# Performance work log

Measured on AMD Instinct MI355X. Metric: run time of the kernel, lower is better.

The kernel has to match this reference:

```python
import jax, jax.numpy as jnp
import numpy as np

ENT_TOTAL = 100000
REL_TOTAL = 1000
HIDDEN = 128
BATCH_SEQ = 8192  # 2 * batch_size (pos + neg halves)
MARGIN = 1.0
LAMB = 0.01
REG = 0.01


def setup_inputs() -> dict:
    key = jax.random.key(0)
    k0, k1, k2 = jax.random.split(key, 3)
    # [batch_seq, 3] index triples (h, r, t); values valid for both tables
    inp = jax.random.randint(k0, (BATCH_SEQ, 3), 0, REL_TOTAL, dtype=jnp.int64)
    # xavier-ish embedding tables
    scale = 1.0 / np.sqrt(HIDDEN)
    ent_emb = jax.random.normal(k1, (ENT_TOTAL, HIDDEN), dtype=jnp.float32) * scale
    rel_emb = jax.random.normal(k2, (REL_TOTAL, HIDDEN), dtype=jnp.float32) * scale
    Wr = jnp.zeros((REL_TOTAL, HIDDEN, HIDDEN), dtype=jnp.float32)
    return {"input": inp, "ent_emb": ent_emb, "rel_emb": rel_emb, "Wr": Wr}


def reference(input, ent_emb, rel_emb, Wr):
    bs = input.shape[0] // 2
    # gather embeddings (torch code keeps a singleton middle dim; we squeeze it)
    h = ent_emb[input[:, 0]]  # [2bs, H]
    r = rel_emb[input[:, 1]]
    t = ent_emb[input[:, 2]]
    error = jnp.abs(h + r - t)  # [2bs, H]
    ep, en = error[:bs], error[bs:]

    # relWr[b] = en_b en_b^T - ep_b ep_b^T  (abs-error outer products)
    relWr = jnp.einsum('bh,bk->bhk', en, en) - jnp.einsum('bh,bk->bhk', ep, ep)

    # matching torch scatter_ nondeterministic overwrite semantics)
    pos_r = input[:bs, 1]
    Wr_new = Wr.at[pos_r].set(relWr)

    # quadratic-form cross scores: p[i, j] = ep_i^T relWr_j ep_j (torch broadcast matmul semantics)
    vp = jnp.einsum('jhk,jk->jh', relWr, ep)  # [bs, H]
    vn = jnp.einsum('jhk,jk->jh', relWr, en)
    p_score = ep @ vp.T  # [bs, bs]
    n_score = en @ vn.T

    margin_loss = jnp.sum(jax.nn.relu(p_score - n_score + MARGIN)) / bs
    wr_loss = jnp.linalg.norm(relWr.reshape(-1)) * LAMB  # Frobenius (p=2) norm
    norm_loss = (jnp.linalg.norm(h.reshape(-1)) + jnp.linalg.norm(r.reshape(-1))
                 + jnp.linalg.norm(t.reshape(-1))) * REG
    loss = margin_loss + wr_loss + norm_loss
    return (loss, Wr_new)
```

## Files before the change

### kernel.cpp

```cpp
#include <hip/hip_runtime.h>
#include <hip/hip_bf16.h>
#include <math.h>

#define HID 128
#define BSEQ 8192
#define BSH 4096
#define RELS 1000
#define KEXT 256

typedef unsigned int u32;
typedef __attribute__((ext_vector_type(8))) short bf16x8;
typedef __attribute__((ext_vector_type(4))) float f32x4;


__device__ inline unsigned short f2bf(float x) {
    u32 u = __float_as_uint(x);
    u32 r = (u + 0x7fff + ((u >> 16) & 1)) >> 16;
    return (unsigned short)r;
}

__device__ inline u32 pack2bf(float x) {
    unsigned short hi = f2bf(x);
    float hf = __uint_as_float((u32)hi << 16);
    unsigned short lo = f2bf(x - hf);
    return (u32)hi | ((u32)lo << 16);
}

#define GLOAD_LDS16(g, l) __builtin_amdgcn_global_load_lds( \
    (const __attribute__((address_space(1))) u32*)(g), \
    (__attribute__((address_space(3))) u32*)(l), 16, 0, 0)

__global__ void k_init(int* __restrict__ winner) {
    int t = blockIdx.x * blockDim.x + threadIdx.x;
    if (t < RELS) winner[t] = -1;
}

__global__ __launch_bounds__(256) void k_prep(const int* __restrict__ idx,
                                              const float* __restrict__ ent,
                                              const float* __restrict__ rel,
                                              float* __restrict__ e,
                                              u32* __restrict__ S,
                                              float* __restrict__ abc,
                                              int* __restrict__ winner,
                                              double* __restrict__ part) {
    const int b = blockIdx.x;
    const int half = threadIdx.x >> 7;
    const int k = threadIdx.x & 127;
    const int row = half ? (b + BSH) : b;
    const int i0 = idx[row * 3 + 0];
    const int i1 = idx[row * 3 + 1];
    const int i2 = idx[row * 3 + 2];
    const float h = ent[(size_t)i0 * HID + k];
    const float r = rel[(size_t)i1 * HID + k];
    const float t = ent[(size_t)i2 * HID + k];
    const float val = fabsf(h + r - t);
    e[(size_t)row * HID + k] = val;

    __shared__ float sE[2][128];
    __shared__ float sh[3][4];
    __shared__ float sPart[3][2];
    sE[half][k] = val;

    float hh = h * h, rr = r * r, tt = t * t;
    #pragma unroll
    for (int off = 32; off; off >>= 1) {
        hh += __shfl_down(hh, off);
        rr += __shfl_down(rr, off);
        tt += __shfl_down(tt, off);
    }
    int lane = threadIdx.x & 63, wv = threadIdx.x >> 6;
    if (lane == 0) { sh[0][wv] = hh; sh[1][wv] = rr; sh[2][wv] = tt; }
    __syncthreads();

    const float p = sE[0][k], n = sE[1][k];
    {
        size_t base = ((size_t)(1 + half) * BSH + b) * (KEXT / 2);
        S[base + k] = pack2bf(val);
        if (half == 0) {
            size_t ub = (size_t)b * (KEXT / 2);
            S[ub + k] = pack2bf(p + n);
        }
    }
    if (half == 0) {
        float ak = p * n, bk = p * p, ck = n * n;
        #pragma unroll
        for (int off = 32; off; off >>= 1) {
            ak += __shfl_down(ak, off);
            bk += __shfl_down(bk, off);
            ck += __shfl_down(ck, off);
        }
        if (lane == 0) { sPart[0][wv] = ak; sPart[1][wv] = bk; sPart[2][wv] = ck; }
    }
    __syncthreads();
    if (threadIdx.x == 0) {
        float a = sPart[0][0] + sPart[0][1];
        float bb = sPart[1][0] + sPart[1][1];
        float c = sPart[2][0] + sPart[2][1];
        abc[b] = a; abc[BSH + b] = bb; abc[2 * BSH + b] = c;
        double ad = a, bd = bb, cd = c;
        part[(size_t)b * 4 + 0] = (double)(sh[0][0] + sh[0][1] + sh[0][2] + sh[0][3]);
        part[(size_t)b * 4 + 1] = (double)(sh[1][0] + sh[1][1] + sh[1][2] + sh[1][3]);
        part[(size_t)b * 4 + 2] = (double)(sh[2][0] + sh[2][1] + sh[2][2] + sh[2][3]);
        part[(size_t)b * 4 + 3] = cd * cd - 2.0 * ad * ad + bd * bd;
        atomicMax(&winner[i1], b);
    }
}

__global__ __launch_bounds__(256) void k_scoremm(const unsigned short* __restrict__ S,
                                                 const float* __restrict__ abc,
                                                 double* __restrict__ pm) {
    int bi = blockIdx.y, bj = blockIdx.x;
    const int flat = bi * 64 + bj;
    if (bj < bi) {
        if (threadIdx.x == 0) pm[flat] = 0.0;
        return;
    }
    const int I0 = bi * 64, J0 = bj * 64;
    __shared__ __align__(16) unsigned short sAll[6 * 64 * 32];
    __shared__ float sRed[4];
    const int t = threadIdx.x;
    const int lane = t & 63, wv = t >> 6;
    const int wr = wv >> 1, wc = wv & 1;
    const int lam = lane & 15, lag = lane >> 4;

    f32x4 a0[2][2] = {}, a1[2][2] = {}, a2[2][2] = {};

    for (int kc = 0; kc < 8; ++kc) {
        __syncthreads();
        #pragma unroll
        for (int qq = 0; qq < 6; ++qq) {
            int q = wv * 6 + qq;
            int b = q * 1024 + lane * 16;
            int arr = b >> 12;
            int within = b & 4095;
            int row = within >> 6;
            int colB = within & 63;
            int m = arr >> 1;
            int R0 = (arr & 1) ? J0 : I0;
            const unsigned short* src = S + ((size_t)(m * BSH + R0 + row) << 8)
                                          + kc * 32 + (colB >> 1);
            GLOAD_LDS16(src, &sAll[q * 512]);
        }
        __syncthreads();
        bf16x8 fa[3][2], fb[3][2];
        #pragma unroll
        for (int m = 0; m < 3; ++m) {
            #pragma unroll
            for (int f = 0; f < 2; ++f) {
                fa[m][f] = *(const bf16x8*)&sAll[(m * 2 + 0) * 2048
                              + (wr * 32 + f * 16 + lam) * 32 + lag * 8];
                fb[m][f] = *(const bf16x8*)&sAll[(m * 2 + 1) * 2048
                              + (wc * 32 + f * 16 + lam) * 32 + lag * 8];
            }
        }
        #pragma unroll
        for (int fi = 0; fi < 2; ++fi)
            #pragma unroll
            for (int fj = 0; fj < 2; ++fj) {
                a0[fi][fj] = __builtin_amdgcn_mfma_f32_16x16x32_bf16(fa[0][fi], fb[0][fj], a0[fi][fj], 0, 0, 0);
                a1[fi][fj] = __builtin_amdgcn_mfma_f32_16x16x32_bf16(fa[1][fi], fb[1][fj], a1[fi][fj], 0, 0, 0);
                a2[fi][fj] = __builtin_amdgcn_mfma_f32_16x16x32_bf16(fa[2][fi], fb[2][fj], a2[fi][fj], 0, 0, 0);
            }
    }

    const float* A = abc;
    const float* Bv = abc + BSH;
    const float* Cv = abc + 2 * BSH;
    float lsum = 0.f;
    #pragma unroll
    for (int fj = 0; fj < 2; ++fj) {
        int j = J0 + wc * 32 + fj * 16 + lam;
        float aj = A[j], abj = aj + Bv[j], acj = aj + Cv[j];
        #pragma unroll
        for (int fi = 0; fi < 2; ++fi)
            #pragma unroll
            for (int r = 0; r < 4; ++r) {
                float s = fmaf(aj, a0[fi][fj][r], 1.0f)
                          - abj * a1[fi][fj][r] - acj * a2[fi][fj][r];
                lsum += fmaxf(s, 0.f);
            }
    }
    if (bj != bi) {
        #pragma unroll
        for (int fi = 0; fi < 2; ++fi)
            #pragma unroll
            for (int r = 0; r < 4; ++r) {
                int i = I0 + wr * 32 + fi * 16 + lag * 4 + r;
                float ai = A[i], abi = ai + Bv[i], aci = ai + Cv[i];
                #pragma unroll
                for (int fj = 0; fj < 2; ++fj) {
                    float s = fmaf(ai, a0[fi][fj][r], 1.0f)
                              - abi * a1[fi][fj][r] - aci * a2[fi][fj][r];
                    lsum += fmaxf(s, 0.f);
                }
            }
    }
    #pragma unroll
    for (int off = 32; off; off >>= 1) lsum += __shfl_down(lsum, off);
    if (lane == 0) sRed[wv] = lsum;
    __syncthreads();
    if (t == 0)
        pm[flat] = (double)(sRed[0] + sRed[1] + sRed[2] + sRed[3]);
}

__global__ __launch_bounds__(256) void k_reduce(const double* __restrict__ pp,
                                                const double* __restrict__ pm,
                                                float* __restrict__ out) {
    int t = threadIdx.x;
    double h2 = 0, r2 = 0, t2 = 0, wr = 0, mg = 0;
    for (int i = t; i < BSH; i += 256) {
        h2 += pp[(size_t)i * 4 + 0];
        r2 += pp[(size_t)i * 4 + 1];
        t2 += pp[(size_t)i * 4 + 2];
        wr += pp[(size_t)i * 4 + 3];
        mg += pm[i];
    }
    #pragma unroll
    for (int off = 32; off; off >>= 1) {
        h2 += __shfl_down(h2, off);
        r2 += __shfl_down(r2, off);
        t2 += __shfl_down(t2, off);
        wr += __shfl_down(wr, off);
        mg += __shfl_down(mg, off);
    }
    __shared__ double sred[5][4];
    int lane = t & 63, wv = t >> 6;
    if (lane == 0) {
        sred[0][wv] = h2; sred[1][wv] = r2; sred[2][wv] = t2;
        sred[3][wv] = wr; sred[4][wv] = mg;
    }
    __syncthreads();
    if (t == 0) {
        double H = sred[0][0] + sred[0][1] + sred[0][2] + sred[0][3];
        double R = sred[1][0] + sred[1][1] + sred[1][2] + sred[1][3];
        double T = sred[2][0] + sred[2][1] + sred[2][2] + sred[2][3];
        double W = sred[3][0] + sred[3][1] + sred[3][2] + sred[3][3];
        double M = sred[4][0] + sred[4][1] + sred[4][2] + sred[4][3];
        out[0] = (float)(M / (double)BSH + sqrt(W) * 0.01
                         + (sqrt(H) + sqrt(R) + sqrt(T)) * 0.01);
    }
}

__global__ __launch_bounds__(256) void k_wrout(const float* __restrict__ Wr,
                                               const float* __restrict__ e,
                                               const int* __restrict__ winner,
                                               float* __restrict__ outWr) {
    int rel = blockIdx.x;
    int t = threadIdx.x;
    float* out = outWr + (size_t)rel * HID * HID;
    int j = winner[rel];
    if (j < 0) {
        const float* src = Wr + (size_t)rel * HID * HID;
        #pragma unroll 8
        for (int it = 0; it < 64; ++it) out[it * 256 + t] = src[it * 256 + t];
    } else {
        __shared__ float sep[HID], sen[HID];
        if (t < 128) sep[t] = e[(size_t)j * HID + t];
        else sen[t - 128] = e[(size_t)(j + BSH) * HID + (t - 128)];
        __syncthreads();
        #pragma unroll 8
        for (int it = 0; it < 64; ++it) {
            int ix = it * 256 + t;
            int hh = ix >> 7, kk = ix & 127;
            out[ix] = sen[hh] * sen[kk] - sep[hh] * sep[kk];
        }
    }
}

extern "C" void kernel_launch(void* const* d_in, const int* in_sizes, int n_in,
                              void* d_out, int out_size, void* d_ws, size_t ws_size,
                              hipStream_t stream) {
    const int* idx = (const int*)d_in[0];
    const float* ent = (const float*)d_in[1];
    const float* rel = (const float*)d_in[2];
    const float* Wr = (const float*)d_in[3];
    float* out = (float*)d_out;

    char* ws = (char*)d_ws;
    int* winner = (int*)(ws + 64);
    float* abc = (float*)(ws + 4096);
    float* e = (float*)(ws + 53248);
    u32* S = (u32*)(out + 4);
    double* pp = (double*)((char*)d_out + 6291488);
    double* pm = (double*)((char*)d_out + 6422560);

    k_init<<<4, 256, 0, stream>>>(winner);
    k_prep<<<BSH, 256, 0, stream>>>(idx, ent, rel, e, S, abc, winner, pp);
    k_scoremm<<<dim3(64, 64), 256, 0, stream>>>((const unsigned short*)S, abc, pm);
    k_reduce<<<1, 256, 0, stream>>>(pp, pm, out);
    k_wrout<<<RELS, 256, 0, stream>>>(Wr, e, winner, out + 1);
}
```

Before: 222.6 us.

## Double-buffer LDS staging in score matmul and launch only upper-triangle tiles

The score GEMM kernel now stages K-chunks into two LDS buffers with explicit vmcnt waits, so the global-to-LDS loads for chunk k+2 overlap the MFMA work on chunk k. The grid is also shrunk from a 64x64 launch, where lower-triangle blocks exited immediately, to a 1D launch of only the 2080 upper-triangle tiles. Each tile's row and column are recovered with a sqrt-based index mapping, and the final reduction reads only those 2080 partials. This doubles LDS use per block and relies on hand-placed waitcnt and barrier ordering for correctness.

Measured after the change: 212.3 us. -4.6%, faster.

```diff
diff --git a/kernel.cpp b/kernel.cpp
--- a/kernel.cpp
+++ b/kernel.cpp
@@ -7,22 +7,25 @@
 #define BSH 4096
 #define RELS 1000
 #define KEXT 256
+#define NTILE 64
+#define NTRI 2080
 
 typedef unsigned int u32;
+typedef unsigned short u16;
 typedef __attribute__((ext_vector_type(8))) short bf16x8;
 typedef __attribute__((ext_vector_type(4))) float f32x4;
 
 
-__device__ inline unsigned short f2bf(float x) {
+__device__ inline u16 f2bf(float x) {
     u32 u = __float_as_uint(x);
     u32 r = (u + 0x7fff + ((u >> 16) & 1)) >> 16;
-    return (unsigned short)r;
+    return (u16)r;
 }
 
 __device__ inline u32 pack2bf(float x) {
-    unsigned short hi = f2bf(x);
+    u16 hi = f2bf(x);
     float hf = __uint_as_float((u32)hi << 16);
-    unsigned short lo = f2bf(x - hf);
+    u16 lo = f2bf(x - hf);
     return (u32)hi | ((u32)lo << 16);
 }
 
@@ -106,17 +109,36 @@
     }
 }
 
-__global__ __launch_bounds__(256) void k_scoremm(const unsigned short* __restrict__ S,
+__device__ __forceinline__ void stage_chunk(const u16* __restrict__ S,
+                                            int I0, int J0, int wv, int lane,
+                                            int kc, u16* lds) {
+    #pragma unroll
+    for (int qq = 0; qq < 6; ++qq) {
+        int q = wv * 6 + qq;
+        int b = q * 1024 + lane * 16;
+        int arr = b >> 12;
+        int within = b & 4095;
+        int row = within >> 6;
+        int colB = within & 63;
+        int m = arr >> 1;
+        int R0 = (arr & 1) ? J0 : I0;
+        const u16* src = S + ((size_t)(m * BSH + R0 + row) << 8)
+                           + kc * 32 + (colB >> 1);
+        GLOAD_LDS16(src, &lds[q * 512]);
+    }
+}
+
+__global__ __launch_bounds__(256) void k_scoremm(const u16* __restrict__ S,
                                                  const float* __restrict__ abc,
                                                  double* __restrict__ pm) {
-    int bi = blockIdx.y, bj = blockIdx.x;
-    const int flat = bi * 64 + bj;
-    if (bj < bi) {
-        if (threadIdx.x == 0) pm[flat] = 0.0;
-        return;
-    }
+    const int f = blockIdx.x;
+    int bi = (int)(64.5f - sqrtf(64.5f * 64.5f - 2.0f * (float)f));
+    while ((bi + 1) * NTILE - ((bi + 1) * bi) / 2 <= f) ++bi;
+    while (bi * NTILE - (bi * (bi - 1)) / 2 > f) --bi;
+    const int bj = bi + (f - (bi * NTILE - (bi * (bi - 1)) / 2));
     const int I0 = bi * 64, J0 = bj * 64;
-    __shared__ __align__(16) unsigned short sAll[6 * 64 * 32];
+
+    __shared__ __align__(16) u16 sAll[2][6 * 64 * 32];
     __shared__ float sRed[4];
     const int t = threadIdx.x;
     const int lane = t & 63, wv = t >> 6;
@@ -125,43 +147,50 @@
 
     f32x4 a0[2][2] = {}, a1[2][2] = {}, a2[2][2] = {};
 
-    for (int kc = 0; kc < 8; ++kc) {
-        __syncthreads();
-        #pragma unroll
-        for (int qq = 0; qq < 6; ++qq) {
-            int q = wv * 6 + qq;
-            int b = q * 1024 + lane * 16;
-            int arr = b >> 12;
-            int within = b & 4095;
-            int row = within >> 6;
-            int colB = within & 63;
-            int m = arr >> 1;
-            int R0 = (arr & 1) ? J0 : I0;
-            const unsigned short* src = S + ((size_t)(m * BSH + R0 + row) << 8)
-                                          + kc * 32 + (colB >> 1);
-            GLOAD_LDS16(src, &sAll[q * 512]);
-        }
-        __syncthreads();
-        bf16x8 fa[3][2], fb[3][2];
-        #pragma unroll
-        for (int m = 0; m < 3; ++m) {
-            #pragma unroll
-            for (int f = 0; f < 2; ++f) {
-                fa[m][f] = *(const bf16x8*)&sAll[(m * 2 + 0) * 2048
-                              + (wr * 32 + f * 16 + lam) * 32 + lag * 8];
-                fb[m][f] = *(const bf16x8*)&sAll[(m * 2 + 1) * 2048
-                              + (wc * 32 + f * 16 + lam) * 32 + lag * 8];
-            }
-        }
-        #pragma unroll
-        for (int fi = 0; fi < 2; ++fi)
-            #pragma unroll
-            for (int fj = 0; fj < 2; ++fj) {
-                a0[fi][fj] = __builtin_amdgcn_mfma_f32_16x16x32_bf16(fa[0][fi], fb[0][fj], a0[fi][fj], 0, 0, 0);
-                a1[fi][fj] = __builtin_amdgcn_mfma_f32_16x16x32_bf16(fa[1][fi], fb[1][fj], a1[fi][fj], 0, 0, 0);
-                a2[fi][fj] = __builtin_amdgcn_mfma_f32_16x16x32_bf16(fa[2][fi], fb[2][fj], a2[fi][fj], 0, 0, 0);
-            }
-    }
+    stage_chunk(S, I0, J0, wv, lane, 0, sAll[0]);
+    stage_chunk(S, I0, J0, wv, lane, 1, sAll[1]);
+
+#define KSTEP(KC, NWAIT)                                                      \
+    {                                                                         \
+        asm volatile("s_waitcnt vmcnt(" #NWAIT ")" ::: "memory");             \
+        __builtin_amdgcn_sched_barrier(0);                                    \
+        __builtin_amdgcn_s_barrier();                                         \
+        __builtin_amdgcn_sched_barrier(0);                                    \
+        const u16* buf = sAll[KC & 1];                                        \
+        bf16x8 fa[3][2], fb[3][2];                                            \
+        _Pragma("unroll")                                                     \
+        for (int m = 0; m < 3; ++m) {                                         \
+            _Pragma("unroll")                                                 \
+            for (int ff = 0; ff < 2; ++ff) {                                  \
+                fa[m][ff] = *(const bf16x8*)&buf[(m * 2 + 0) * 2048           \
+                               + (wr * 32 + ff * 16 + lam) * 32 + lag * 8];   \
+                fb[m][ff] = *(const bf16x8*)&buf[(m * 2 + 1) * 2048           \
+                               + (wc * 32 + ff * 16 + lam) * 32 + lag * 8];   \
+            }                                                                 \
+        }                                                                     \
+        asm volatile("s_waitcnt lgkmcnt(0)" ::: "memory");                    \
+        __builtin_amdgcn_sched_barrier(0);                                    \
+        __builtin_amdgcn_s_barrier();                                         \
+        __builtin_amdgcn_sched_barrier(0);                                    \
+        if ((KC) + 2 < 8)                                                     \
+            stage_chunk(S, I0, J0, wv, lane, (KC) + 2, sAll[KC & 1]);         \
+        _Pragma("unroll")                                                     \
+        for (int fi = 0; fi < 2; ++fi) {                                      \
+            _Pragma("unroll")                                                 \
+            for (int fj = 0; fj < 2; ++fj) {                                  \
+                a0[fi][fj] = __builtin_amdgcn_mfma_f32_16x16x32_bf16(         \
+                    fa[0][fi], fb[0][fj], a0[fi][fj], 0, 0, 0);               \
+                a1[fi][fj] = __builtin_amdgcn_mfma_f32_16x16x32_bf16(         \
+                    fa[1][fi], fb[1][fj], a1[fi][fj], 0, 0, 0);               \
+                a2[fi][fj] = __builtin_amdgcn_mfma_f32_16x16x32_bf16(         \
+                    fa[2][fi], fb[2][fj], a2[fi][fj], 0, 0, 0);               \
+            }                                                                 \
+        }                                                                     \
+    }
+
+    KSTEP(0, 6) KSTEP(1, 6) KSTEP(2, 6) KSTEP(3, 6)
+    KSTEP(4, 6) KSTEP(5, 6) KSTEP(6, 6) KSTEP(7, 0)
+#undef KSTEP
 
     const float* A = abc;
     const float* Bv = abc + BSH;
@@ -200,7 +229,7 @@
     if (lane == 0) sRed[wv] = lsum;
     __syncthreads();
     if (t == 0)
-        pm[flat] = (double)(sRed[0] + sRed[1] + sRed[2] + sRed[3]);
+        pm[f] = (double)(sRed[0] + sRed[1] + sRed[2] + sRed[3]);
 }
 
 __global__ __launch_bounds__(256) void k_reduce(const double* __restrict__ pp,
@@ -213,7 +242,7 @@
         r2 += pp[(size_t)i * 4 + 1];
         t2 += pp[(size_t)i * 4 + 2];
         wr += pp[(size_t)i * 4 + 3];
-        mg += pm[i];
+        if (i < NTRI) mg += pm[i];
     }
     #pragma unroll
     for (int off = 32; off; off >>= 1) {
@@ -286,7 +315,7 @@
 
     k_init<<<4, 256, 0, stream>>>(winner);
     k_prep<<<BSH, 256, 0, stream>>>(idx, ent, rel, e, S, abc, winner, pp);
-    k_scoremm<<<dim3(64, 64), 256, 0, stream>>>((const unsigned short*)S, abc, pm);
+    k_scoremm<<<NTRI, 256, 0, stream>>>((const u16*)S, abc, pm);
     k_reduce<<<1, 256, 0, stream>>>(pp, pm, out);
     k_wrout<<<RELS, 256, 0, stream>>>(Wr, e, winner, out + 1);
 }
```

## Load MFMA fragments directly from global via fragment-friendly layout, launch triangular grid

Applied to the files above, without the earlier changes.

The packed bf16 operand array is rewritten in a k-chunk-major layout, so each lane's 8-element MFMA fragment is a contiguous 16-byte global load. The score kernel drops the LDS staging and both barriers per k-step and reads fragments straight into registers. The grid now launches only the 2080 upper-triangular tiles instead of 4096 blocks, half of which exited early, with an interleaved tile order and a closed-form index mapping. This removes LDS traffic and empty blocks, but loses the data sharing through LDS, so each wave fetches its own operands from global/L2.

Measured after the change: 207.3 us. 6.8% less time.

```diff
diff --git a/kernel.cpp b/kernel.cpp
--- a/kernel.cpp
+++ b/kernel.cpp
@@ -6,29 +6,28 @@
 #define BSEQ 8192
 #define BSH 4096
 #define RELS 1000
-#define KEXT 256
+#define NTILE 64
+#define NTRI 2080
+#define PSTRIDE 524288
 
 typedef unsigned int u32;
+typedef unsigned short u16;
 typedef __attribute__((ext_vector_type(8))) short bf16x8;
 typedef __attribute__((ext_vector_type(4))) float f32x4;
 
 
-__device__ inline unsigned short f2bf(float x) {
+__device__ inline u16 f2bf(float x) {
     u32 u = __float_as_uint(x);
     u32 r = (u + 0x7fff + ((u >> 16) & 1)) >> 16;
-    return (unsigned short)r;
+    return (u16)r;
 }
 
 __device__ inline u32 pack2bf(float x) {
-    unsigned short hi = f2bf(x);
+    u16 hi = f2bf(x);
     float hf = __uint_as_float((u32)hi << 16);
-    unsigned short lo = f2bf(x - hf);
+    u16 lo = f2bf(x - hf);
     return (u32)hi | ((u32)lo << 16);
 }
-
-#define GLOAD_LDS16(g, l) __builtin_amdgcn_global_load_lds( \
-    (const __attribute__((address_space(1))) u32*)(g), \
-    (__attribute__((address_space(3))) u32*)(l), 16, 0, 0)
 
 __global__ void k_init(int* __restrict__ winner) {
     int t = blockIdx.x * blockDim.x + threadIdx.x;
@@ -74,12 +73,9 @@
 
     const float p = sE[0][k], n = sE[1][k];
     {
-        size_t base = ((size_t)(1 + half) * BSH + b) * (KEXT / 2);
-        S[base + k] = pack2bf(val);
-        if (half == 0) {
-            size_t ub = (size_t)b * (KEXT / 2);
-            S[ub + k] = pack2bf(p + n);
-        }
+        size_t kidx = ((size_t)(k >> 2) * BSH + b) * 4 + (k & 3);
+        S[(size_t)(1 + half) * PSTRIDE + kidx] = pack2bf(val);
+        if (half == 0) S[kidx] = pack2bf(p + n);
     }
     if (half == 0) {
         float ak = p * n, bk = p * p, ck = n * n;
@@ -106,60 +102,51 @@
     }
 }
 
-__global__ __launch_bounds__(256) void k_scoremm(const unsigned short* __restrict__ S,
+__global__ __launch_bounds__(256) void k_scoremm(const u32* __restrict__ S,
                                                  const float* __restrict__ abc,
                                                  double* __restrict__ pm) {
-    int bi = blockIdx.y, bj = blockIdx.x;
-    const int flat = bi * 64 + bj;
-    if (bj < bi) {
-        if (threadIdx.x == 0) pm[flat] = 0.0;
-        return;
-    }
+    const int bid = blockIdx.x;
+    const int f = (bid & 7) * (NTRI / 8) + (bid >> 3);
+    int bi = (int)(64.5f - sqrtf(64.5f * 64.5f - 2.0f * (float)f));
+    while ((bi + 1) * NTILE - ((bi + 1) * bi) / 2 <= f) ++bi;
+    while (bi * NTILE - (bi * (bi - 1)) / 2 > f) --bi;
+    const int bj = bi + (f - (bi * NTILE - (bi * (bi - 1)) / 2));
     const int I0 = bi * 64, J0 = bj * 64;
-    __shared__ __align__(16) unsigned short sAll[6 * 64 * 32];
+
     __shared__ float sRed[4];
     const int t = threadIdx.x;
     const int lane = t & 63, wv = t >> 6;
     const int wr = wv >> 1, wc = wv & 1;
     const int lam = lane & 15, lag = lane >> 4;
 
+    const u32* baseA = S + ((size_t)lag * BSH + I0 + wr * 32 + lam) * 4;
+    const u32* baseB = S + ((size_t)lag * BSH + J0 + wc * 32 + lam) * 4;
+
     f32x4 a0[2][2] = {}, a1[2][2] = {}, a2[2][2] = {};
 
+    #pragma unroll
     for (int kc = 0; kc < 8; ++kc) {
-        __syncthreads();
-        #pragma unroll
-        for (int qq = 0; qq < 6; ++qq) {
-            int q = wv * 6 + qq;
-            int b = q * 1024 + lane * 16;
-            int arr = b >> 12;
-            int within = b & 4095;
-            int row = within >> 6;
-            int colB = within & 63;
-            int m = arr >> 1;
-            int R0 = (arr & 1) ? J0 : I0;
-            const unsigned short* src = S + ((size_t)(m * BSH + R0 + row) << 8)
-                                          + kc * 32 + (colB >> 1);
-            GLOAD_LDS16(src, &sAll[q * 512]);
+        bf16x8 fa[3][2], fb[3][2];
+        #pragma unroll
+        for (int m = 0; m < 3; ++m) {
+            #pragma unroll
+            for (int ff = 0; ff < 2; ++ff) {
+                fa[m][ff] = *(const bf16x8*)(baseA + (size_t)m * PSTRIDE
+                                             + kc * 65536 + ff * 64);
+                fb[m][ff] = *(const bf16x8*)(baseB + (size_t)m * PSTRIDE
+                                             + kc * 65536 + ff * 64);
+            }
         }
-        __syncthreads();
-        bf16x8 fa[3][2], fb[3][2];
-        #pragma unroll
-        for (int m = 0; m < 3; ++m) {
-            #pragma unroll
-            for (int f = 0; f < 2; ++f) {
-                fa[m][f] = *(const bf16x8*)&sAll[(m * 2 + 0) * 2048
-                              + (wr * 32 + f * 16 + lam) * 32 + lag * 8];
-                fb[m][f] = *(const bf16x8*)&sAll[(m * 2 + 1) * 2048
-                              + (wc * 32 + f * 16 + lam) * 32 + lag * 8];
-            }
-        }
         #pragma unroll
         for (int fi = 0; fi < 2; ++fi)
             #pragma unroll
             for (int fj = 0; fj < 2; ++fj) {
-                a0[fi][fj] = __builtin_amdgcn_mfma_f32_16x16x32_bf16(fa[0][fi], fb[0][fj], a0[fi][fj], 0, 0, 0);
-                a1[fi][fj] = __builtin_amdgcn_mfma_f32_16x16x32_bf16(fa[1][fi], fb[1][fj], a1[fi][fj], 0, 0, 0);
-                a2[fi][fj] = __builtin_amdgcn_mfma_f32_16x16x32_bf16(fa[2][fi], fb[2][fj], a2[fi][fj], 0, 0, 0);
+                a0[fi][fj] = __builtin_amdgcn_mfma_f32_16x16x32_bf16(
+                    fa[0][fi], fb[0][fj], a0[fi][fj], 0, 0, 0);
+                a1[fi][fj] = __builtin_amdgcn_mfma_f32_16x16x32_bf16(
+                    fa[1][fi], fb[1][fj], a1[fi][fj], 0, 0, 0);
+                a2[fi][fj] = __builtin_amdgcn_mfma_f32_16x16x32_bf16(
+                    fa[2][fi], fb[2][fj], a2[fi][fj], 0, 0, 0);
             }
     }
 
@@ -200,7 +187,7 @@
     if (lane == 0) sRed[wv] = lsum;
     __syncthreads();
     if (t == 0)
-        pm[flat] = (double)(sRed[0] + sRed[1] + sRed[2] + sRed[3]);
+        pm[f] = (double)(sRed[0] + sRed[1] + sRed[2] + sRed[3]);
 }
 
 __global__ __launch_bounds__(256) void k_reduce(const double* __restrict__ pp,
@@ -213,7 +200,7 @@
         r2 += pp[(size_t)i * 4 + 1];
         t2 += pp[(size_t)i * 4 + 2];
         wr += pp[(size_t)i * 4 + 3];
-        mg += pm[i];
+        if (i < NTRI) mg += pm[i];
     }
     #pragma unroll
     for (int off = 32; off; off >>= 1) {
@@ -286,7 +273,7 @@
 
     k_init<<<4, 256, 0, stream>>>(winner);
     k_prep<<<BSH, 256, 0, stream>>>(idx, ent, rel, e, S, abc, winner, pp);
-    k_scoremm<<<dim3(64, 64), 256, 0, stream>>>((const unsigned short*)S, abc, pm);
+    k_scoremm<<<NTRI, 256, 0, stream>>>(S, abc, pm);
     k_reduce<<<1, 256, 0, stream>>>(pp, pm, out);
     k_wrout<<<RELS, 256, 0, stream>>>(Wr, e, winner, out + 1);
 }
```
